# Kernel tuning notes

Measured on AMD Instinct MI355X. Metric: run time of the kernel, lower is better.

## Reference

```python
import jax, jax.numpy as jnp
import numpy as np

N, E = 50000, 400000
HID, EDGE, NRBF = 128, 16, 32
CUTOFF = 5.0
EPS = 1e-8


def setup_inputs() -> dict:
    key = jax.random.key(0)
    ks = jax.random.split(key, 16)
    s = lambda fan_in: 1.0 / np.sqrt(fan_in)
    mlp_in = 3 * HID + NRBF + EDGE  # 432
    return {
        "h": jax.random.normal(ks[0], (N, HID), jnp.float32),
        "vec": jax.random.normal(ks[1], (N, 3, HID), jnp.float32),
        "coord": jax.random.normal(ks[2], (N, 3), jnp.float32),
        "edge_index": jax.random.randint(ks[3], (2, E), 0, N, jnp.int32),
        "edge_attr": jax.random.normal(ks[4], (E, EDGE), jnp.float32),
        "Wvp": jax.random.normal(ks[5], (HID, 3 * HID), jnp.float32) * s(HID),
        "W1": jax.random.normal(ks[6], (mlp_in, HID), jnp.float32) * s(mlp_in),
        "b1": jnp.zeros((HID,), jnp.float32),
        "W2": jax.random.normal(ks[7], (HID, HID), jnp.float32) * s(HID),
        "b2": jnp.zeros((HID,), jnp.float32),
        "W3": jax.random.normal(ks[8], (HID, 3 * HID), jnp.float32) * s(HID),
        "b3": jnp.zeros((3 * HID,), jnp.float32),
        "Wop": jax.random.normal(ks[9], (HID, 3 * HID), jnp.float32) * s(HID),
        "bop": jnp.zeros((3 * HID,), jnp.float32),
    }


def _rbf(d):
    # Gaussian smearing: centers on linspace(0, cutoff, n_rbf)
    offsets = jnp.linspace(0.0, CUTOFF, NRBF, dtype=d.dtype)
    coeff = -0.5 / (offsets[1] - offsets[0]) ** 2
    return jnp.exp(coeff * (d[:, None] - offsets) ** 2)  # [E, NRBF]


def reference(h, vec, coord, edge_index, edge_attr,
              Wvp, W1, b1, W2, b2, W3, b3, Wop, bop):
    row, col = edge_index[0], edge_index[1]
    x_ij = coord[row] - coord[col]                          # [E,3]
    d = jnp.sqrt(jnp.sum(x_ij * x_ij, axis=-1) + EPS)       # stable_norm
    d_ij = _rbf(d)                                          # [E,NRBF]

    vecp = jnp.einsum('nvh,hk->nvk', vec, Wvp)              # [N,3,3H]
    vec1, vec2, vec3 = jnp.split(vecp, 3, axis=-1)          # each [N,3,H]
    vec_dot = jnp.sum(vec1 * vec2, axis=1)                  # [N,H]

    cross = jnp.sum(vec1[row] * vec2[col], axis=1)          # [E,H]
    mlp_in = jnp.concatenate([h[row], h[col], d_ij, cross, edge_attr], axis=-1)
    x = jax.nn.silu(mlp_in @ W1 + b1)
    x = jax.nn.silu(x @ W2 + b2)
    msg = x @ W3 + b3                                       # [E,3H]
    msg_h, msg_v, msg_x = jnp.split(msg, 3, axis=1)

    h_aggr = jax.ops.segment_sum(msg_h, row, num_segments=N)           # [N,H]
    vec_msg = vec3[col] * msg_v[:, None, :] + msg_x[:, None, :] * x_ij[:, :, None]
    vec_aggr = jax.ops.segment_sum(vec_msg, row, num_segments=N)       # [N,3,H]

    o = h_aggr @ Wop + bop
    o1, o2, o3 = jnp.split(o, 3, axis=1)
    dh = vec_dot * o2 + o3
    dvec = vec3 * o1[:, None, :] + vec_aggr
    return dh, dvec
```

## Files before the change

### kernel.cpp

```cpp
#include <hip/hip_runtime.h>
#include <math.h>

constexpr int NN    = 50000;
constexpr int NE    = 400000;
constexpr int HID   = 128;

constexpr size_t OFF_VECP = 0;
constexpr size_t OFF_HAGG = 57600000;
constexpr size_t OFF_HW   = 64000000;
constexpr size_t OFF_WT   = 83200000;
constexpr size_t OFF_PERM = 83421184;
constexpr size_t OFF_DEG  = 83821184;
constexpr size_t OFF_CUR  = 83871184;
constexpr size_t WS_FLOATS = 83921184;

constexpr size_t O_HWH = 0;
constexpr size_t O_HWL = 32768;
constexpr size_t O_W1H = 65536;
constexpr size_t O_W1L = 90112;
constexpr size_t O_W2H = 114688;
constexpr size_t O_W2L = 131072;
constexpr size_t O_W3H = 147456;
constexpr size_t O_W3L = 196608;
constexpr size_t O_VPH = 245760;
constexpr size_t O_VPL = 294912;
constexpr size_t O_OPH = 344064;
constexpr size_t O_OPL = 393216;

typedef __attribute__((ext_vector_type(8))) short short8;
typedef __attribute__((ext_vector_type(4))) float f32x4;

__device__ __forceinline__ short f2bf_rne(float f) {
    unsigned u = __float_as_uint(f);
    u += 0x7fffu + ((u >> 16) & 1u);
    return (short)(u >> 16);
}
__device__ __forceinline__ float bf2f(short h) {
    return __uint_as_float(((unsigned)(unsigned short)h) << 16);
}
__device__ __forceinline__ void split8(const float* t, short8& ah, short8& al) {
#pragma unroll
    for (int j = 0; j < 8; ++j) {
        short hi = f2bf_rne(t[j]);
        ah[j] = hi;
        al[j] = f2bf_rne(t[j] - bf2f(hi));
    }
}
__device__ __forceinline__ f32x4 mfma4(short8 ah, short8 al, short8 bh, short8 bl, f32x4 c) {
    c = __builtin_amdgcn_mfma_f32_16x16x32_bf16(ah, bh, c, 0, 0, 0);
    c = __builtin_amdgcn_mfma_f32_16x16x32_bf16(al, bh, c, 0, 0, 0);
    c = __builtin_amdgcn_mfma_f32_16x16x32_bf16(ah, bl, c, 0, 0, 0);
    c = __builtin_amdgcn_mfma_f32_16x16x32_bf16(al, bl, c, 0, 0, 0);
    return c;
}

#define VLOAD8(dst, src) do { \
    *(float4*)&(dst)[0] = *(const float4*)(src); \
    *(float4*)&(dst)[4] = *(const float4*)((src) + 4); } while (0)

__global__ void misc_kernel(const float* __restrict__ W1, const float* __restrict__ W2,
                            const float* __restrict__ W3, const float* __restrict__ Wvp,
                            const float* __restrict__ Wop, short* __restrict__ wt,
                            const int* __restrict__ eidx, int* __restrict__ deg,
                            float* __restrict__ hagg, float* __restrict__ dvec)
{
    const int bid = blockIdx.x;
    const int idx = bid * 256 + threadIdx.x;
    {
        int n = idx >> 7, k = idx & 127;
        hagg[idx] = 0.f;
        size_t db = (size_t)n * 384 + k;
        dvec[db] = 0.f; dvec[db + 128] = 0.f; dvec[db + 256] = 0.f;
    }
    if (bid < 864) {
        float v; size_t oh, ol;
        if (idx < 32768) {
            int j = idx >> 7, k = idx & 127;
            v = (j < 128) ? W1[(size_t)k * 128 + j] : W1[(size_t)(128 + k) * 128 + (j - 128)];
            oh = O_HWH + idx; ol = O_HWL + idx;
        } else if (idx < 57344) {
            int l = idx - 32768; int n = l / 192, k = l - n * 192;
            int r = (k < 128) ? (288 + k) : (k < 160) ? (256 + k - 128) : (k < 176) ? (416 + k - 160) : -1;
            v = (r < 0) ? 0.f : W1[(size_t)r * 128 + n];
            oh = O_W1H + l; ol = O_W1L + l;
        } else if (idx < 73728) {
            int l = idx - 57344; int n = l >> 7, k = l & 127;
            v = W2[(size_t)k * 128 + n];
            oh = O_W2H + l; ol = O_W2L + l;
        } else if (idx < 122880) {
            int l = idx - 73728; int n = l >> 7, k = l & 127;
            v = W3[(size_t)k * 384 + n];
            oh = O_W3H + l; ol = O_W3L + l;
        } else if (idx < 172032) {
            int l = idx - 122880; int n = l >> 7, k = l & 127;
            v = Wvp[(size_t)k * 384 + n];
            oh = O_VPH + l; ol = O_VPL + l;
        } else {
            int l = idx - 172032; int n = l >> 7, k = l & 127;
            v = Wop[(size_t)k * 384 + n];
            oh = O_OPH + l; ol = O_OPL + l;
        }
        short hi = f2bf_rne(v);
        wt[oh] = hi;
        wt[ol] = f2bf_rne(v - bf2f(hi));
    }
    if (bid < 1563 && idx < NE)
        atomicAdd(&deg[eidx[idx]], 1);
}

__global__ void __launch_bounds__(1024)
sort_scan(const int* __restrict__ deg, int* __restrict__ cursor)
{
    __shared__ int part[1024];
    const int tid = threadIdx.x;
    const int base = tid * 49;
    int s = 0;
#pragma unroll 7
    for (int j = 0; j < 49; ++j) {
        int i = base + j;
        if (i < NN) s += deg[i];
    }
    part[tid] = s;
    __syncthreads();
    for (int off = 1; off < 1024; off <<= 1) {
        int v = (tid >= off) ? part[tid - off] : 0;
        __syncthreads();
        part[tid] += v;
        __syncthreads();
    }
    int run = part[tid] - s;
    for (int j = 0; j < 49; ++j) {
        int i = base + j;
        if (i < NN) { cursor[i] = run; run += deg[i]; }
    }
}

__global__ void sort_scatter(const int* __restrict__ eidx, int* __restrict__ cursor,
                             int* __restrict__ perm)
{
    int e = blockIdx.x * 256 + threadIdx.x;
    if (e < NE) {
        int pos = atomicAdd(&cursor[eidx[e]], 1);
        perm[pos] = e;
    }
}

template<int NT>
__global__ void __launch_bounds__(256, 3)
gemm_node(const float* __restrict__ A, int M,
          const short* __restrict__ wh, const short* __restrict__ wl,
          float* __restrict__ C, const float* __restrict__ bias)
{
    const int N = NT * 64;
    const int tid = threadIdx.x, wave = tid >> 6, lane = tid & 63;
    const int m = lane & 15, kg = lane >> 4;
    const int gm0 = blockIdx.x * 32;
    const int nb = wave * NT * 16;
    const f32x4 zf = {0.f, 0.f, 0.f, 0.f};
    f32x4 acc[2][NT];
#pragma unroll
    for (int mt = 0; mt < 2; ++mt)
#pragma unroll
        for (int tt = 0; tt < NT; ++tt) acc[mt][tt] = zf;

    for (int ks = 0; ks < 4; ++ks) {
        short8 ah[2], al[2];
#pragma unroll
        for (int mt = 0; mt < 2; ++mt) {
            int r = gm0 + mt * 16 + m;
            if (r >= M) r = M - 1;
            float tmp[8];
            VLOAD8(tmp, A + (size_t)r * 128 + ks * 32 + kg * 8);
            split8(tmp, ah[mt], al[mt]);
        }
#pragma unroll
        for (int tt = 0; tt < NT; ++tt) {
            size_t wo = (size_t)(nb + tt * 16 + m) * 128 + ks * 32 + kg * 8;
            short8 bh = *(const short8*)(wh + wo);
            short8 bl = *(const short8*)(wl + wo);
#pragma unroll
            for (int mt = 0; mt < 2; ++mt)
                acc[mt][tt] = mfma4(ah[mt], al[mt], bh, bl, acc[mt][tt]);
        }
    }
    float bv[NT];
#pragma unroll
    for (int tt = 0; tt < NT; ++tt) bv[tt] = bias ? bias[nb + tt * 16 + m] : 0.f;
#pragma unroll
    for (int mt = 0; mt < 2; ++mt)
#pragma unroll
        for (int r = 0; r < 4; ++r) {
            int row = gm0 + mt * 16 + kg * 4 + r;
            if (row < M) {
#pragma unroll
                for (int tt = 0; tt < NT; ++tt)
                    C[(size_t)row * N + nb + tt * 16 + m] = acc[mt][tt][r] + bv[tt];
            }
        }
}

__global__ void __launch_bounds__(256, 3)
gemm_fin(const float* __restrict__ hagg, const float* __restrict__ vecp,
         const short* __restrict__ wh, const short* __restrict__ wl,
         const float* __restrict__ bop, float* __restrict__ dh,
         float* __restrict__ dvec, int M)
{
    const int tid = threadIdx.x, wave = tid >> 6, lane = tid & 63;
    const int m = lane & 15, kg = lane >> 4;
    const int gm0 = blockIdx.x * 32;
    const int nb = wave * 32;
    const f32x4 zf = {0.f, 0.f, 0.f, 0.f};
    f32x4 acc[2][6];
#pragma unroll
    for (int mt = 0; mt < 2; ++mt)
#pragma unroll
        for (int t = 0; t < 6; ++t) acc[mt][t] = zf;

    for (int ks = 0; ks < 4; ++ks) {
        short8 ah[2], al[2];
#pragma unroll
        for (int mt = 0; mt < 2; ++mt) {
            int r = gm0 + mt * 16 + m;
            if (r >= M) r = M - 1;
            float tmp[8];
            VLOAD8(tmp, hagg + (size_t)r * 128 + ks * 32 + kg * 8);
            split8(tmp, ah[mt], al[mt]);
        }
#pragma unroll
        for (int seg = 0; seg < 3; ++seg)
#pragma unroll
            for (int tt = 0; tt < 2; ++tt) {
                size_t wo = (size_t)(seg * 128 + nb + tt * 16 + m) * 128 + ks * 32 + kg * 8;
                short8 bh = *(const short8*)(wh + wo);
                short8 bl = *(const short8*)(wl + wo);
#pragma unroll
                for (int mt = 0; mt < 2; ++mt)
                    acc[mt][seg * 2 + tt] = mfma4(ah[mt], al[mt], bh, bl, acc[mt][seg * 2 + tt]);
            }
    }
    float bo[3][2];
#pragma unroll
    for (int seg = 0; seg < 3; ++seg)
#pragma unroll
        for (int tt = 0; tt < 2; ++tt) bo[seg][tt] = bop[seg * 128 + nb + tt * 16 + m];

#pragma unroll
    for (int mt = 0; mt < 2; ++mt)
#pragma unroll
        for (int r = 0; r < 4; ++r) {
            int row = gm0 + mt * 16 + kg * 4 + r;
            if (row >= M) continue;
            size_t b = (size_t)row * 1152;
#pragma unroll
            for (int tt = 0; tt < 2; ++tt) {
                int k = nb + tt * 16 + m;
                float o1 = acc[mt][0 * 2 + tt][r] + bo[0][tt];
                float o2 = acc[mt][1 * 2 + tt][r] + bo[1][tt];
                float o3 = acc[mt][2 * 2 + tt][r] + bo[2][tt];
                float vd = vecp[b + k]       * vecp[b + 128 + k]
                         + vecp[b + 384 + k] * vecp[b + 512 + k]
                         + vecp[b + 768 + k] * vecp[b + 896 + k];
                dh[(size_t)row * 128 + k] = vd * o2 + o3;
                size_t db = (size_t)row * 384 + k;
                dvec[db]       += vecp[b + 256 + k]  * o1;
                dvec[db + 128] += vecp[b + 640 + k]  * o1;
                dvec[db + 256] += vecp[b + 1024 + k] * o1;
            }
        }
}

__global__ void __launch_bounds__(256, 4)
edge_kernel(const float* __restrict__ vecp, const float* __restrict__ hw,
            const float* __restrict__ coord, const int* __restrict__ eidx,
            const float* __restrict__ eattr, const short* __restrict__ wt,
            const int* __restrict__ perm,
            const float* __restrict__ b1, const float* __restrict__ b2,
            const float* __restrict__ b3,
            float* __restrict__ hagg, float* __restrict__ dvec)
{
    __shared__ __align__(16) unsigned char smem[34816];
    short (*abh)[40]  = (short(*)[40])(&smem[0]);
    short (*abl)[40]  = (short(*)[40])(&smem[5120]);
    short (*xh)[136]  = (short(*)[136])(&smem[0]);
    short (*xl)[136]  = (short(*)[136])(&smem[17408]);
    __shared__ int   s_row[64], s_col[64], s_es[64];
    __shared__ float s_xij[64][3];
    __shared__ float s_d[64];

    const int tid = threadIdx.x;
    const int wave = tid >> 6, lane = tid & 63;
    const int m = lane & 15, kg = lane >> 4;
    const int nb = wave * 32;
    const int eb = blockIdx.x * 64;
    const int be = tid >> 2;
    const int bq = (tid & 3) * 8;

    if (tid < 64) {
        int es = perm[eb + tid];
        int r = eidx[es], c = eidx[NE + es];
        s_es[tid] = es; s_row[tid] = r; s_col[tid] = c;
        float x0 = coord[r * 3 + 0] - coord[c * 3 + 0];
        float x1 = coord[r * 3 + 1] - coord[c * 3 + 1];
        float x2 = coord[r * 3 + 2] - coord[c * 3 + 2];
        s_xij[tid][0] = x0; s_xij[tid][1] = x1; s_xij[tid][2] = x2;
        s_d[tid] = sqrtf(x0 * x0 + x1 * x1 + x2 * x2 + 1e-8f);
    }
    __syncthreads();

    const f32x4 zf = {0.f, 0.f, 0.f, 0.f};
    const float delta = 5.0f / 31.0f;
    const float coeff = -0.5f / (delta * delta);
    const int brow = s_row[be], bcol = s_col[be], bes = s_es[be];

    float pA[8], pB[8], pC[8], pD[8], pE[8], pF[8];
    auto issue = [&](int ks) {
        if (ks < 4) {
            int kk = ks * 32 + bq;
            const float* vr = vecp + (size_t)brow * 1152 + kk;
            const float* vc = vecp + (size_t)bcol * 1152 + 128 + kk;
            VLOAD8(pA, vr);       VLOAD8(pB, vc);
            VLOAD8(pC, vr + 384); VLOAD8(pD, vc + 384);
            VLOAD8(pE, vr + 768); VLOAD8(pF, vc + 768);
        } else if (ks == 5) {
            if (bq < 16) VLOAD8(pA, eattr + (size_t)bes * 16 + bq);
        }
    };
    auto commit = [&](int ks) {
        float tmp[8];
        if (ks < 4) {
#pragma unroll
            for (int j = 0; j < 8; ++j)
                tmp[j] = pA[j] * pB[j] + pC[j] * pD[j] + pE[j] * pF[j];
        } else if (ks == 4) {
            float dd = s_d[be];
#pragma unroll
            for (int j = 0; j < 8; ++j) {
                float x = dd - (float)(bq + j) * delta;
                tmp[j] = __expf(coeff * x * x);
            }
        } else {
#pragma unroll
            for (int j = 0; j < 8; ++j) tmp[j] = (bq < 16) ? pA[j] : 0.f;
        }
        short8 sh, sl; split8(tmp, sh, sl);
        *(short8*)&abh[be][bq] = sh;
        *(short8*)&abl[be][bq] = sl;
    };

    f32x4 acc[4][2];
#pragma unroll
    for (int mt = 0; mt < 4; ++mt) { acc[mt][0] = zf; acc[mt][1] = zf; }

    issue(0); commit(0);
    __syncthreads();
    for (int ks = 0; ks < 6; ++ks) {
        if (ks < 5) issue(ks + 1);
        short8 ah4[4], al4[4];
#pragma unroll
        for (int mt = 0; mt < 4; ++mt) {
            ah4[mt] = *(const short8*)&abh[mt * 16 + m][kg * 8];
            al4[mt] = *(const short8*)&abl[mt * 16 + m][kg * 8];
        }
#pragma unroll
        for (int tt = 0; tt < 2; ++tt) {
            size_t wo = (size_t)(nb + tt * 16 + m) * 192 + ks * 32 + kg * 8;
            short8 bh = *(const short8*)(wt + O_W1H + wo);
            short8 bl = *(const short8*)(wt + O_W1L + wo);
#pragma unroll
            for (int mt = 0; mt < 4; ++mt)
                acc[mt][tt] = mfma4(ah4[mt], al4[mt], bh, bl, acc[mt][tt]);
        }
        __syncthreads();
        if (ks < 5) { commit(ks + 1); __syncthreads(); }
    }

    {
        float b1v[2] = { b1[nb + m], b1[nb + 16 + m] };
#pragma unroll
        for (int mt = 0; mt < 4; ++mt) {
            float hb[4][4];
#pragma unroll
            for (int r = 0; r < 4; ++r) {
                int e = mt * 16 + kg * 4 + r;
                const float* hr = hw + (size_t)s_row[e] * 256;
                const float* hc = hw + (size_t)s_col[e] * 256 + 128;
                hb[r][0] = hr[nb + m];      hb[r][1] = hc[nb + m];
                hb[r][2] = hr[nb + 16 + m]; hb[r][3] = hc[nb + 16 + m];
            }
#pragma unroll
            for (int r = 0; r < 4; ++r) {
                int e = mt * 16 + kg * 4 + r;
#pragma unroll
                for (int tt = 0; tt < 2; ++tt) {
                    int n = nb + tt * 16 + m;
                    float v = acc[mt][tt][r] + hb[r][tt * 2] + hb[r][tt * 2 + 1] + b1v[tt];
                    float sv = v * __builtin_amdgcn_rcpf(1.f + __expf(-v));
                    short hi = f2bf_rne(sv);
                    xh[e][n] = hi;
                    xl[e][n] = f2bf_rne(sv - bf2f(hi));
                }
            }
        }
    }
    __syncthreads();

#pragma unroll
    for (int mt = 0; mt < 4; ++mt) { acc[mt][0] = zf; acc[mt][1] = zf; }
    for (int ks = 0; ks < 4; ++ks) {
        short8 ah4[4], al4[4];
#pragma unroll
        for (int mt = 0; mt < 4; ++mt) {
            ah4[mt] = *(const short8*)&xh[mt * 16 + m][ks * 32 + kg * 8];
            al4[mt] = *(const short8*)&xl[mt * 16 + m][ks * 32 + kg * 8];
        }
#pragma unroll
        for (int tt = 0; tt < 2; ++tt) {
            size_t wo = (size_t)(nb + tt * 16 + m) * 128 + ks * 32 + kg * 8;
            short8 bh = *(const short8*)(wt + O_W2H + wo);
            short8 bl = *(const short8*)(wt + O_W2L + wo);
#pragma unroll
            for (int mt = 0; mt < 4; ++mt)
                acc[mt][tt] = mfma4(ah4[mt], al4[mt], bh, bl, acc[mt][tt]);
        }
    }
    {
        float b2v[2] = { b2[nb + m], b2[nb + 16 + m] };
#pragma unroll
        for (int mt = 0; mt < 4; ++mt)
#pragma unroll
            for (int tt = 0; tt < 2; ++tt)
#pragma unroll
                for (int r = 0; r < 4; ++r) {
                    float v = acc[mt][tt][r] + b2v[tt];
                    acc[mt][tt][r] = v * __builtin_amdgcn_rcpf(1.f + __expf(-v));
                }
    }
    __syncthreads();
#pragma unroll
    for (int mt = 0; mt < 4; ++mt)
#pragma unroll
        for (int tt = 0; tt < 2; ++tt)
#pragma unroll
            for (int r = 0; r < 4; ++r) {
                int e = mt * 16 + kg * 4 + r;
                int n = nb + tt * 16 + m;
                float sv = acc[mt][tt][r];
                short hi = f2bf_rne(sv);
                xh[e][n] = hi;
                xl[e][n] = f2bf_rne(sv - bf2f(hi));
            }
    __syncthreads();

    float msgv[4][2][4];
    for (int c = 0; c < 3; ++c) {
        f32x4 a3[4][2];
#pragma unroll
        for (int mt = 0; mt < 4; ++mt) { a3[mt][0] = zf; a3[mt][1] = zf; }
        for (int ks = 0; ks < 4; ++ks) {
            short8 ah4[4], al4[4];
#pragma unroll
            for (int mt = 0; mt < 4; ++mt) {
                ah4[mt] = *(const short8*)&xh[mt * 16 + m][ks * 32 + kg * 8];
                al4[mt] = *(const short8*)&xl[mt * 16 + m][ks * 32 + kg * 8];
            }
#pragma unroll
            for (int tt = 0; tt < 2; ++tt) {
                size_t wo = (size_t)(c * 128 + nb + tt * 16 + m) * 128 + ks * 32 + kg * 8;
                short8 bh = *(const short8*)(wt + O_W3H + wo);
                short8 bl = *(const short8*)(wt + O_W3L + wo);
#pragma unroll
                for (int mt = 0; mt < 4; ++mt)
                    a3[mt][tt] = mfma4(ah4[mt], al4[mt], bh, bl, a3[mt][tt]);
            }
        }
        float bv[2] = { b3[c * 128 + nb + m], b3[c * 128 + nb + 16 + m] };
        const int n0 = nb + m, n1 = nb + 16 + m;
        if (c == 0) {
            int cur = s_row[kg * 4];
            float s0 = 0.f, s1 = 0.f;
#pragma unroll
            for (int mt = 0; mt < 4; ++mt)
#pragma unroll
                for (int r = 0; r < 4; ++r) {
                    int rr = s_row[mt * 16 + kg * 4 + r];
                    float v0 = a3[mt][0][r] + bv[0];
                    float v1 = a3[mt][1][r] + bv[1];
                    if (rr != cur) {
                        atomicAdd(&hagg[(size_t)cur * 128 + n0], s0);
                        atomicAdd(&hagg[(size_t)cur * 128 + n1], s1);
                        cur = rr; s0 = 0.f; s1 = 0.f;
                    }
                    s0 += v0; s1 += v1;
                }
            atomicAdd(&hagg[(size_t)cur * 128 + n0], s0);
            atomicAdd(&hagg[(size_t)cur * 128 + n1], s1);
        } else if (c == 1) {
#pragma unroll
            for (int mt = 0; mt < 4; ++mt)
#pragma unroll
                for (int tt = 0; tt < 2; ++tt)
#pragma unroll
                    for (int r = 0; r < 4; ++r)
                        msgv[mt][tt][r] = a3[mt][tt][r] + bv[tt];
        } else {
            int cur = s_row[kg * 4];
            float sd[6] = {0.f, 0.f, 0.f, 0.f, 0.f, 0.f};
#pragma unroll
            for (int mt = 0; mt < 4; ++mt) {
                float v3b[4][6];
#pragma unroll
                for (int r = 0; r < 4; ++r) {
                    int e = mt * 16 + kg * 4 + r;
                    const float* v3 = vecp + (size_t)s_col[e] * 1152 + 256;
                    v3b[r][0] = v3[n0]; v3b[r][1] = v3[384 + n0]; v3b[r][2] = v3[768 + n0];
                    v3b[r][3] = v3[n1]; v3b[r][4] = v3[384 + n1]; v3b[r][5] = v3[768 + n1];
                }
#pragma unroll
                for (int r = 0; r < 4; ++r) {
                    int e = mt * 16 + kg * 4 + r;
                    int rr = s_row[e];
                    if (rr != cur) {
                        float* dst = dvec + (size_t)cur * 384;
                        atomicAdd(dst + n0,       sd[0]);
                        atomicAdd(dst + 128 + n0, sd[1]);
                        atomicAdd(dst + 256 + n0, sd[2]);
                        atomicAdd(dst + n1,       sd[3]);
                        atomicAdd(dst + 128 + n1, sd[4]);
                        atomicAdd(dst + 256 + n1, sd[5]);
                        cur = rr;
#pragma unroll
                        for (int q = 0; q < 6; ++q) sd[q] = 0.f;
                    }
                    const float xj0 = s_xij[e][0], xj1 = s_xij[e][1], xj2 = s_xij[e][2];
                    float mx0 = a3[mt][0][r] + bv[0], mx1 = a3[mt][1][r] + bv[1];
                    float mv0 = msgv[mt][0][r],       mv1 = msgv[mt][1][r];
                    sd[0] += v3b[r][0] * mv0 + xj0 * mx0;
                    sd[1] += v3b[r][1] * mv0 + xj1 * mx0;
                    sd[2] += v3b[r][2] * mv0 + xj2 * mx0;
                    sd[3] += v3b[r][3] * mv1 + xj0 * mx1;
                    sd[4] += v3b[r][4] * mv1 + xj1 * mx1;
                    sd[5] += v3b[r][5] * mv1 + xj2 * mx1;
                }
            }
            float* dst = dvec + (size_t)cur * 384;
            atomicAdd(dst + n0,       sd[0]);
            atomicAdd(dst + 128 + n0, sd[1]);
            atomicAdd(dst + 256 + n0, sd[2]);
            atomicAdd(dst + n1,       sd[3]);
            atomicAdd(dst + 128 + n1, sd[4]);
            atomicAdd(dst + 256 + n1, sd[5]);
        }
    }
}

extern "C" void kernel_launch(void* const* d_in, const int* in_sizes, int n_in,
                              void* d_out, int out_size, void* d_ws, size_t ws_size,
                              hipStream_t stream)
{
    const float* h     = (const float*)d_in[0];
    const float* vec   = (const float*)d_in[1];
    const float* coord = (const float*)d_in[2];
    const int*   eidx  = (const int*)  d_in[3];
    const float* eattr = (const float*)d_in[4];
    const float* Wvp   = (const float*)d_in[5];
    const float* W1    = (const float*)d_in[6];
    const float* b1    = (const float*)d_in[7];
    const float* W2    = (const float*)d_in[8];
    const float* b2    = (const float*)d_in[9];
    const float* W3    = (const float*)d_in[10];
    const float* b3    = (const float*)d_in[11];
    const float* Wop   = (const float*)d_in[12];
    const float* bop   = (const float*)d_in[13];

    if (ws_size < WS_FLOATS * sizeof(float)) return;

    float* ws   = (float*)d_ws;
    float* vecp = ws + OFF_VECP;
    float* hagg = ws + OFF_HAGG;
    float* hw   = ws + OFF_HW;
    short* wt   = (short*)(ws + OFF_WT);
    int*   perm = (int*)(ws + OFF_PERM);
    int*   deg  = (int*)(ws + OFF_DEG);
    int*   cur  = (int*)(ws + OFF_CUR);
    float* dh   = (float*)d_out;
    float* dvec = (float*)d_out + (size_t)NN * HID;

    dim3 b256(256);
    hipMemsetAsync(deg, 0, NN * sizeof(int), stream);
    misc_kernel<<<25000, b256, 0, stream>>>(W1, W2, W3, Wvp, Wop, wt, eidx, deg, hagg, dvec);
    sort_scan<<<1, 1024, 0, stream>>>(deg, cur);
    sort_scatter<<<1563, b256, 0, stream>>>(eidx, cur, perm);
    gemm_node<6><<<4688, b256, 0, stream>>>(vec, 150000, wt + O_VPH, wt + O_VPL, vecp, nullptr);
    gemm_node<4><<<1563, b256, 0, stream>>>(h, 50000, wt + O_HWH, wt + O_HWL, hw, nullptr);
    edge_kernel<<<6250, b256, 0, stream>>>(vecp, hw, coord, eidx, eattr, wt, perm,
                                           b1, b2, b3, hagg, dvec);
    gemm_fin<<<1563, b256, 0, stream>>>(hagg, vecp, wt + O_OPH, wt + O_OPL, bop, dh, dvec, 50000);
}
```

Before: 1.340 ms.

## Halve edge tile to 32 edges per block and double-buffer first-layer staging

Result: slower. 1.668 ms (+24.5%).

```diff
diff --git a/kernel.cpp b/kernel.cpp
--- a/kernel.cpp
+++ b/kernel.cpp
@@ -28,6 +28,7 @@
 constexpr size_t O_OPL = 393216;
 
 typedef __attribute__((ext_vector_type(8))) short short8;
+typedef __attribute__((ext_vector_type(4))) short s16x4;
 typedef __attribute__((ext_vector_type(4))) float f32x4;
 
 __device__ __forceinline__ short f2bf_rne(float f) {
@@ -41,6 +42,14 @@
 __device__ __forceinline__ void split8(const float* t, short8& ah, short8& al) {
 #pragma unroll
     for (int j = 0; j < 8; ++j) {
+        short hi = f2bf_rne(t[j]);
+        ah[j] = hi;
+        al[j] = f2bf_rne(t[j] - bf2f(hi));
+    }
+}
+__device__ __forceinline__ void split4(const float* t, s16x4& ah, s16x4& al) {
+#pragma unroll
+    for (int j = 0; j < 4; ++j) {
         short hi = f2bf_rne(t[j]);
         ah[j] = hi;
         al[j] = f2bf_rne(t[j] - bf2f(hi));
@@ -57,6 +66,8 @@
 #define VLOAD8(dst, src) do { \
     *(float4*)&(dst)[0] = *(const float4*)(src); \
     *(float4*)&(dst)[4] = *(const float4*)((src) + 4); } while (0)
+#define VLOAD4(dst, src) do { \
+    *(float4*)&(dst)[0] = *(const float4*)(src); } while (0)
 
 __global__ void misc_kernel(const float* __restrict__ W1, const float* __restrict__ W2,
                             const float* __restrict__ W3, const float* __restrict__ Wvp,
@@ -269,7 +280,7 @@
         }
 }
 
-__global__ void __launch_bounds__(256, 4)
+__global__ void __launch_bounds__(256, 8)
 edge_kernel(const float* __restrict__ vecp, const float* __restrict__ hw,
             const float* __restrict__ coord, const int* __restrict__ eidx,
             const float* __restrict__ eattr, const short* __restrict__ wt,
@@ -278,24 +289,22 @@
             const float* __restrict__ b3,
             float* __restrict__ hagg, float* __restrict__ dvec)
 {
-    __shared__ __align__(16) unsigned char smem[34816];
-    short (*abh)[40]  = (short(*)[40])(&smem[0]);
-    short (*abl)[40]  = (short(*)[40])(&smem[5120]);
-    short (*xh)[136]  = (short(*)[136])(&smem[0]);
-    short (*xl)[136]  = (short(*)[136])(&smem[17408]);
-    __shared__ int   s_row[64], s_col[64], s_es[64];
-    __shared__ float s_xij[64][3];
-    __shared__ float s_d[64];
+    __shared__ __align__(16) unsigned char smem[17408];
+    short (*xh)[136] = (short(*)[136])(&smem[0]);
+    short (*xl)[136] = (short(*)[136])(&smem[8704]);
+    __shared__ int   s_row[32], s_col[32], s_es[32];
+    __shared__ float s_xij[32][3];
+    __shared__ float s_d[32];
 
     const int tid = threadIdx.x;
     const int wave = tid >> 6, lane = tid & 63;
     const int m = lane & 15, kg = lane >> 4;
     const int nb = wave * 32;
-    const int eb = blockIdx.x * 64;
-    const int be = tid >> 2;
-    const int bq = (tid & 3) * 8;
-
-    if (tid < 64) {
+    const int eb = blockIdx.x * 32;
+    const int be = tid >> 3;
+    const int bq = (tid & 7) * 4;
+
+    if (tid < 32) {
         int es = perm[eb + tid];
         int r = eidx[es], c = eidx[NE + es];
         s_es[tid] = es; s_row[tid] = r; s_col[tid] = c;
@@ -312,54 +321,58 @@
     const float coeff = -0.5f / (delta * delta);
     const int brow = s_row[be], bcol = s_col[be], bes = s_es[be];
 
-    float pA[8], pB[8], pC[8], pD[8], pE[8], pF[8];
+    float pA[4], pB[4], pC[4], pD[4], pE[4], pF[4];
     auto issue = [&](int ks) {
         if (ks < 4) {
             int kk = ks * 32 + bq;
             const float* vr = vecp + (size_t)brow * 1152 + kk;
             const float* vc = vecp + (size_t)bcol * 1152 + 128 + kk;
-            VLOAD8(pA, vr);       VLOAD8(pB, vc);
-            VLOAD8(pC, vr + 384); VLOAD8(pD, vc + 384);
-            VLOAD8(pE, vr + 768); VLOAD8(pF, vc + 768);
+            VLOAD4(pA, vr);       VLOAD4(pB, vc);
+            VLOAD4(pC, vr + 384); VLOAD4(pD, vc + 384);
+            VLOAD4(pE, vr + 768); VLOAD4(pF, vc + 768);
         } else if (ks == 5) {
-            if (bq < 16) VLOAD8(pA, eattr + (size_t)bes * 16 + bq);
+            if (bq < 16) VLOAD4(pA, eattr + (size_t)bes * 16 + bq);
         }
     };
-    auto commit = [&](int ks) {
-        float tmp[8];
+    auto commit = [&](int ks, int buf) {
+        short (*cabh)[40] = (short(*)[40])(&smem[(size_t)buf * 2560]);
+        short (*cabl)[40] = (short(*)[40])(&smem[5120 + (size_t)buf * 2560]);
+        float tmp[4];
         if (ks < 4) {
 #pragma unroll
-            for (int j = 0; j < 8; ++j)
+            for (int j = 0; j < 4; ++j)
                 tmp[j] = pA[j] * pB[j] + pC[j] * pD[j] + pE[j] * pF[j];
         } else if (ks == 4) {
             float dd = s_d[be];
 #pragma unroll
-            for (int j = 0; j < 8; ++j) {
+            for (int j = 0; j < 4; ++j) {
                 float x = dd - (float)(bq + j) * delta;
                 tmp[j] = __expf(coeff * x * x);
             }
         } else {
 #pragma unroll
-            for (int j = 0; j < 8; ++j) tmp[j] = (bq < 16) ? pA[j] : 0.f;
-        }
-        short8 sh, sl; split8(tmp, sh, sl);
-        *(short8*)&abh[be][bq] = sh;
-        *(short8*)&abl[be][bq] = sl;
+            for (int j = 0; j < 4; ++j) tmp[j] = (bq < 16) ? pA[j] : 0.f;
+        }
+        s16x4 sh, sl; split4(tmp, sh, sl);
+        *(s16x4*)&cabh[be][bq] = sh;
+        *(s16x4*)&cabl[be][bq] = sl;
     };
 
-    f32x4 acc[4][2];
-#pragma unroll
-    for (int mt = 0; mt < 4; ++mt) { acc[mt][0] = zf; acc[mt][1] = zf; }
-
-    issue(0); commit(0);
+    f32x4 acc[2][2];
+#pragma unroll
+    for (int mt = 0; mt < 2; ++mt) { acc[mt][0] = zf; acc[mt][1] = zf; }
+
+    issue(0); commit(0, 0);
     __syncthreads();
     for (int ks = 0; ks < 6; ++ks) {
         if (ks < 5) issue(ks + 1);
-        short8 ah4[4], al4[4];
-#pragma unroll
-        for (int mt = 0; mt < 4; ++mt) {
-            ah4[mt] = *(const short8*)&abh[mt * 16 + m][kg * 8];
-            al4[mt] = *(const short8*)&abl[mt * 16 + m][kg * 8];
+        const short (*rabh)[40] = (const short(*)[40])(&smem[(size_t)(ks & 1) * 2560]);
+        const short (*rabl)[40] = (const short(*)[40])(&smem[5120 + (size_t)(ks & 1) * 2560]);
+        short8 ah4[2], al4[2];
+#pragma unroll
+        for (int mt = 0; mt < 2; ++mt) {
+            ah4[mt] = *(const short8*)&rabh[mt * 16 + m][kg * 8];
+            al4[mt] = *(const short8*)&rabl[mt * 16 + m][kg * 8];
         }
 #pragma unroll
         for (int tt = 0; tt < 2; ++tt) {
@@ -367,17 +380,17 @@
             short8 bh = *(const short8*)(wt + O_W1H + wo);
             short8 bl = *(const short8*)(wt + O_W1L + wo);
 #pragma unroll
-            for (int mt = 0; mt < 4; ++mt)
+            for (int mt = 0; mt < 2; ++mt)
                 acc[mt][tt] = mfma4(ah4[mt], al4[mt], bh, bl, acc[mt][tt]);
         }
+        if (ks < 5) commit(ks + 1, (ks + 1) & 1);
         __syncthreads();
-        if (ks < 5) { commit(ks + 1); __syncthreads(); }
     }
 
     {
         float b1v[2] = { b1[nb + m], b1[nb + 16 + m] };
 #pragma unroll
-        for (int mt = 0; mt < 4; ++mt) {
+        for (int mt = 0; mt < 2; ++mt) {
             float hb[4][4];
 #pragma unroll
             for (int r = 0; r < 4; ++r) {
@@ -405,11 +418,11 @@
     __syncthreads();
 
 #pragma unroll
-    for (int mt = 0; mt < 4; ++mt) { acc[mt][0] = zf; acc[mt][1] = zf; }
+    for (int mt = 0; mt < 2; ++mt) { acc[mt][0] = zf; acc[mt][1] = zf; }
     for (int ks = 0; ks < 4; ++ks) {
-        short8 ah4[4], al4[4];
-#pragma unroll
-        for (int mt = 0; mt < 4; ++mt) {
+        short8 ah4[2], al4[2];
+#pragma unroll
+        for (int mt = 0; mt < 2; ++mt) {
             ah4[mt] = *(const short8*)&xh[mt * 16 + m][ks * 32 + kg * 8];
             al4[mt] = *(const short8*)&xl[mt * 16 + m][ks * 32 + kg * 8];
         }
@@ -419,14 +432,14 @@
             short8 bh = *(const short8*)(wt + O_W2H + wo);
             short8 bl = *(const short8*)(wt + O_W2L + wo);
 #pragma unroll
-            for (int mt = 0; mt < 4; ++mt)
+            for (int mt = 0; mt < 2; ++mt)
                 acc[mt][tt] = mfma4(ah4[mt], al4[mt], bh, bl, acc[mt][tt]);
         }
     }
     {
         float b2v[2] = { b2[nb + m], b2[nb + 16 + m] };
 #pragma unroll
-        for (int mt = 0; mt < 4; ++mt)
+        for (int mt = 0; mt < 2; ++mt)
 #pragma unroll
             for (int tt = 0; tt < 2; ++tt)
 #pragma unroll
@@ -437,7 +450,7 @@
     }
     __syncthreads();
 #pragma unroll
-    for (int mt = 0; mt < 4; ++mt)
+    for (int mt = 0; mt < 2; ++mt)
 #pragma unroll
         for (int tt = 0; tt < 2; ++tt)
 #pragma unroll
@@ -451,15 +464,15 @@
             }
     __syncthreads();
 
-    float msgv[4][2][4];
+    float msgv[2][2][4];
     for (int c = 0; c < 3; ++c) {
-        f32x4 a3[4][2];
-#pragma unroll
-        for (int mt = 0; mt < 4; ++mt) { a3[mt][0] = zf; a3[mt][1] = zf; }
+        f32x4 a3[2][2];
+#pragma unroll
+        for (int mt = 0; mt < 2; ++mt) { a3[mt][0] = zf; a3[mt][1] = zf; }
         for (int ks = 0; ks < 4; ++ks) {
-            short8 ah4[4], al4[4];
-#pragma unroll
-            for (int mt = 0; mt < 4; ++mt) {
+            short8 ah4[2], al4[2];
+#pragma unroll
+            for (int mt = 0; mt < 2; ++mt) {
                 ah4[mt] = *(const short8*)&xh[mt * 16 + m][ks * 32 + kg * 8];
                 al4[mt] = *(const short8*)&xl[mt * 16 + m][ks * 32 + kg * 8];
             }
@@ -469,7 +482,7 @@
                 short8 bh = *(const short8*)(wt + O_W3H + wo);
                 short8 bl = *(const short8*)(wt + O_W3L + wo);
 #pragma unroll
-                for (int mt = 0; mt < 4; ++mt)
+                for (int mt = 0; mt < 2; ++mt)
                     a3[mt][tt] = mfma4(ah4[mt], al4[mt], bh, bl, a3[mt][tt]);
             }
         }
@@ -479,7 +492,7 @@
             int cur = s_row[kg * 4];
             float s0 = 0.f, s1 = 0.f;
 #pragma unroll
-            for (int mt = 0; mt < 4; ++mt)
+            for (int mt = 0; mt < 2; ++mt)
 #pragma unroll
                 for (int r = 0; r < 4; ++r) {
                     int rr = s_row[mt * 16 + kg * 4 + r];
@@ -496,7 +509,7 @@
             atomicAdd(&hagg[(size_t)cur * 128 + n1], s1);
         } else if (c == 1) {
 #pragma unroll
-            for (int mt = 0; mt < 4; ++mt)
+            for (int mt = 0; mt < 2; ++mt)
 #pragma unroll
                 for (int tt = 0; tt < 2; ++tt)
 #pragma unroll
@@ -506,7 +519,7 @@
             int cur = s_row[kg * 4];
             float sd[6] = {0.f, 0.f, 0.f, 0.f, 0.f, 0.f};
 #pragma unroll
-            for (int mt = 0; mt < 4; ++mt) {
+            for (int mt = 0; mt < 2; ++mt) {
                 float v3b[4][6];
 #pragma unroll
                 for (int r = 0; r < 4; ++r) {
@@ -592,7 +605,7 @@
     sort_scatter<<<1563, b256, 0, stream>>>(eidx, cur, perm);
     gemm_node<6><<<4688, b256, 0, stream>>>(vec, 150000, wt + O_VPH, wt + O_VPL, vecp, nullptr);
     gemm_node<4><<<1563, b256, 0, stream>>>(h, 50000, wt + O_HWH, wt + O_HWL, hw, nullptr);
-    edge_kernel<<<6250, b256, 0, stream>>>(vecp, hw, coord, eidx, eattr, wt, perm,
-                                           b1, b2, b3, hagg, dvec);
+    edge_kernel<<<12500, b256, 0, stream>>>(vecp, hw, coord, eidx, eattr, wt, perm,
+                                            b1, b2, b3, hagg, dvec);
     gemm_fin<<<1563, b256, 0, stream>>>(hagg, vecp, wt + O_OPH, wt + O_OPL, bop, dh, dvec, 50000);
 }
```

## Store gathered node features as bf16 bundle, double-buffer edge LDS, remap blocks per XCD

Applied to the files above, without the earlier changes.

Result: faster. 1.289 ms (-3.8%).

```diff
diff --git a/kernel.cpp b/kernel.cpp
--- a/kernel.cpp
+++ b/kernel.cpp
@@ -5,9 +5,9 @@
 constexpr int NE    = 400000;
 constexpr int HID   = 128;
 
-constexpr size_t OFF_VECP = 0;
-constexpr size_t OFF_HAGG = 57600000;
-constexpr size_t OFF_HW   = 64000000;
+constexpr size_t OFF_VECP12 = 0;
+constexpr size_t OFF_BUN  = 38400000;
+constexpr size_t OFF_HAGG = 64000000;
 constexpr size_t OFF_WT   = 83200000;
 constexpr size_t OFF_PERM = 83421184;
 constexpr size_t OFF_DEG  = 83821184;
@@ -145,23 +145,21 @@
     }
 }
 
-template<int NT>
 __global__ void __launch_bounds__(256, 3)
-gemm_node(const float* __restrict__ A, int M,
-          const short* __restrict__ wh, const short* __restrict__ wl,
-          float* __restrict__ C, const float* __restrict__ bias)
-{
-    const int N = NT * 64;
+gemm_vp(const float* __restrict__ A, int M,
+        const short* __restrict__ wh, const short* __restrict__ wl,
+        float* __restrict__ vecp12, short* __restrict__ bun)
+{
     const int tid = threadIdx.x, wave = tid >> 6, lane = tid & 63;
     const int m = lane & 15, kg = lane >> 4;
     const int gm0 = blockIdx.x * 32;
-    const int nb = wave * NT * 16;
+    const int nb = wave * 96;
     const f32x4 zf = {0.f, 0.f, 0.f, 0.f};
-    f32x4 acc[2][NT];
+    f32x4 acc[2][6];
 #pragma unroll
     for (int mt = 0; mt < 2; ++mt)
 #pragma unroll
-        for (int tt = 0; tt < NT; ++tt) acc[mt][tt] = zf;
+        for (int tt = 0; tt < 6; ++tt) acc[mt][tt] = zf;
 
     for (int ks = 0; ks < 4; ++ks) {
         short8 ah[2], al[2];
@@ -174,7 +172,7 @@
             split8(tmp, ah[mt], al[mt]);
         }
 #pragma unroll
-        for (int tt = 0; tt < NT; ++tt) {
+        for (int tt = 0; tt < 6; ++tt) {
             size_t wo = (size_t)(nb + tt * 16 + m) * 128 + ks * 32 + kg * 8;
             short8 bh = *(const short8*)(wh + wo);
             short8 bl = *(const short8*)(wl + wo);
@@ -183,24 +181,86 @@
                 acc[mt][tt] = mfma4(ah[mt], al[mt], bh, bl, acc[mt][tt]);
         }
     }
-    float bv[NT];
-#pragma unroll
-    for (int tt = 0; tt < NT; ++tt) bv[tt] = bias ? bias[nb + tt * 16 + m] : 0.f;
 #pragma unroll
     for (int mt = 0; mt < 2; ++mt)
 #pragma unroll
         for (int r = 0; r < 4; ++r) {
             int row = gm0 + mt * 16 + kg * 4 + r;
-            if (row < M) {
-#pragma unroll
-                for (int tt = 0; tt < NT; ++tt)
-                    C[(size_t)row * N + nb + tt * 16 + m] = acc[mt][tt][r] + bv[tt];
+            if (row >= M) continue;
+            int n = row / 3, v = row - n * 3;
+            size_t fb = (size_t)n * 768 + (size_t)v * 256;
+            size_t b2 = (size_t)n * 1024 + (size_t)v * 128;
+            size_t b3 = (size_t)n * 1024 + 384 + (size_t)v * 128;
+#pragma unroll
+            for (int tt = 0; tt < 6; ++tt) {
+                int col = nb + tt * 16 + m;
+                float val = acc[mt][tt][r];
+                int seg = col >> 7, k = col & 127;
+                if (seg == 0) {
+                    vecp12[fb + k] = val;
+                } else if (seg == 1) {
+                    vecp12[fb + 128 + k] = val;
+                    bun[b2 + k] = f2bf_rne(val);
+                } else {
+                    bun[b3 + k] = f2bf_rne(val);
+                }
             }
         }
 }
 
 __global__ void __launch_bounds__(256, 3)
-gemm_fin(const float* __restrict__ hagg, const float* __restrict__ vecp,
+gemm_hw(const float* __restrict__ A, int M,
+        const short* __restrict__ wh, const short* __restrict__ wl,
+        short* __restrict__ bun)
+{
+    const int tid = threadIdx.x, wave = tid >> 6, lane = tid & 63;
+    const int m = lane & 15, kg = lane >> 4;
+    const int gm0 = blockIdx.x * 32;
+    const int nb = wave * 64;
+    const f32x4 zf = {0.f, 0.f, 0.f, 0.f};
+    f32x4 acc[2][4];
+#pragma unroll
+    for (int mt = 0; mt < 2; ++mt)
+#pragma unroll
+        for (int tt = 0; tt < 4; ++tt) acc[mt][tt] = zf;
+
+    for (int ks = 0; ks < 4; ++ks) {
+        short8 ah[2], al[2];
+#pragma unroll
+        for (int mt = 0; mt < 2; ++mt) {
+            int r = gm0 + mt * 16 + m;
+            if (r >= M) r = M - 1;
+            float tmp[8];
+            VLOAD8(tmp, A + (size_t)r * 128 + ks * 32 + kg * 8);
+            split8(tmp, ah[mt], al[mt]);
+        }
+#pragma unroll
+        for (int tt = 0; tt < 4; ++tt) {
+            size_t wo = (size_t)(nb + tt * 16 + m) * 128 + ks * 32 + kg * 8;
+            short8 bh = *(const short8*)(wh + wo);
+            short8 bl = *(const short8*)(wl + wo);
+#pragma unroll
+            for (int mt = 0; mt < 2; ++mt)
+                acc[mt][tt] = mfma4(ah[mt], al[mt], bh, bl, acc[mt][tt]);
+        }
+    }
+#pragma unroll
+    for (int mt = 0; mt < 2; ++mt)
+#pragma unroll
+        for (int r = 0; r < 4; ++r) {
+            int row = gm0 + mt * 16 + kg * 4 + r;
+            if (row >= M) continue;
+#pragma unroll
+            for (int tt = 0; tt < 4; ++tt) {
+                int col = nb + tt * 16 + m;
+                bun[(size_t)row * 1024 + 768 + col] = f2bf_rne(acc[mt][tt][r]);
+            }
+        }
+}
+
+__global__ void __launch_bounds__(256, 3)
+gemm_fin(const float* __restrict__ hagg, const float* __restrict__ vecp12,
+         const short* __restrict__ bun,
          const short* __restrict__ wh, const short* __restrict__ wl,
          const float* __restrict__ bop, float* __restrict__ dh,
          float* __restrict__ dvec, int M)
@@ -250,27 +310,28 @@
         for (int r = 0; r < 4; ++r) {
             int row = gm0 + mt * 16 + kg * 4 + r;
             if (row >= M) continue;
-            size_t b = (size_t)row * 1152;
+            size_t b = (size_t)row * 768;
+            size_t bb = (size_t)row * 1024 + 384;
 #pragma unroll
             for (int tt = 0; tt < 2; ++tt) {
                 int k = nb + tt * 16 + m;
                 float o1 = acc[mt][0 * 2 + tt][r] + bo[0][tt];
                 float o2 = acc[mt][1 * 2 + tt][r] + bo[1][tt];
                 float o3 = acc[mt][2 * 2 + tt][r] + bo[2][tt];
-                float vd = vecp[b + k]       * vecp[b + 128 + k]
-                         + vecp[b + 384 + k] * vecp[b + 512 + k]
-                         + vecp[b + 768 + k] * vecp[b + 896 + k];
+                float vd = vecp12[b + k]       * vecp12[b + 128 + k]
+                         + vecp12[b + 256 + k] * vecp12[b + 384 + k]
+                         + vecp12[b + 512 + k] * vecp12[b + 640 + k];
                 dh[(size_t)row * 128 + k] = vd * o2 + o3;
                 size_t db = (size_t)row * 384 + k;
-                dvec[db]       += vecp[b + 256 + k]  * o1;
-                dvec[db + 128] += vecp[b + 640 + k]  * o1;
-                dvec[db + 256] += vecp[b + 1024 + k] * o1;
+                dvec[db]       += bf2f(bun[bb + k])       * o1;
+                dvec[db + 128] += bf2f(bun[bb + 128 + k]) * o1;
+                dvec[db + 256] += bf2f(bun[bb + 256 + k]) * o1;
             }
         }
 }
 
 __global__ void __launch_bounds__(256, 4)
-edge_kernel(const float* __restrict__ vecp, const float* __restrict__ hw,
+edge_kernel(const float* __restrict__ vecp12, const short* __restrict__ bun,
             const float* __restrict__ coord, const int* __restrict__ eidx,
             const float* __restrict__ eattr, const short* __restrict__ wt,
             const int* __restrict__ perm,
@@ -279,19 +340,22 @@
             float* __restrict__ hagg, float* __restrict__ dvec)
 {
     __shared__ __align__(16) unsigned char smem[34816];
-    short (*abh)[40]  = (short(*)[40])(&smem[0]);
-    short (*abl)[40]  = (short(*)[40])(&smem[5120]);
     short (*xh)[136]  = (short(*)[136])(&smem[0]);
     short (*xl)[136]  = (short(*)[136])(&smem[17408]);
     __shared__ int   s_row[64], s_col[64], s_es[64];
     __shared__ float s_xij[64][3];
     __shared__ float s_d[64];
 
+    const int nwg = gridDim.x;
+    const int q8 = nwg >> 3, r8 = nwg & 7;
+    const int xcd = blockIdx.x & 7, loc = blockIdx.x >> 3;
+    const int lb = (xcd < r8 ? xcd * (q8 + 1) : r8 * (q8 + 1) + (xcd - r8) * q8) + loc;
+
     const int tid = threadIdx.x;
     const int wave = tid >> 6, lane = tid & 63;
     const int m = lane & 15, kg = lane >> 4;
     const int nb = wave * 32;
-    const int eb = blockIdx.x * 64;
+    const int eb = lb * 64;
     const int be = tid >> 2;
     const int bq = (tid & 3) * 8;
 
@@ -312,25 +376,29 @@
     const float coeff = -0.5f / (delta * delta);
     const int brow = s_row[be], bcol = s_col[be], bes = s_es[be];
 
-    float pA[8], pB[8], pC[8], pD[8], pE[8], pF[8];
+    float pA[8], pC[8], pE[8];
+    short8 bB, bD, bF;
     auto issue = [&](int ks) {
         if (ks < 4) {
             int kk = ks * 32 + bq;
-            const float* vr = vecp + (size_t)brow * 1152 + kk;
-            const float* vc = vecp + (size_t)bcol * 1152 + 128 + kk;
-            VLOAD8(pA, vr);       VLOAD8(pB, vc);
-            VLOAD8(pC, vr + 384); VLOAD8(pD, vc + 384);
-            VLOAD8(pE, vr + 768); VLOAD8(pF, vc + 768);
+            const float* vr = vecp12 + (size_t)brow * 768 + kk;
+            const short* vc = bun + (size_t)bcol * 1024 + kk;
+            VLOAD8(pA, vr); VLOAD8(pC, vr + 256); VLOAD8(pE, vr + 512);
+            bB = *(const short8*)(vc);
+            bD = *(const short8*)(vc + 128);
+            bF = *(const short8*)(vc + 256);
         } else if (ks == 5) {
             if (bq < 16) VLOAD8(pA, eattr + (size_t)bes * 16 + bq);
         }
     };
-    auto commit = [&](int ks) {
+    auto commit = [&](int ks, int buf) {
+        short (*cabh)[40] = (short(*)[40])(&smem[(size_t)buf * 5120]);
+        short (*cabl)[40] = (short(*)[40])(&smem[10240 + (size_t)buf * 5120]);
         float tmp[8];
         if (ks < 4) {
 #pragma unroll
             for (int j = 0; j < 8; ++j)
-                tmp[j] = pA[j] * pB[j] + pC[j] * pD[j] + pE[j] * pF[j];
+                tmp[j] = pA[j] * bf2f(bB[j]) + pC[j] * bf2f(bD[j]) + pE[j] * bf2f(bF[j]);
         } else if (ks == 4) {
             float dd = s_d[be];
 #pragma unroll
@@ -343,23 +411,25 @@
             for (int j = 0; j < 8; ++j) tmp[j] = (bq < 16) ? pA[j] : 0.f;
         }
         short8 sh, sl; split8(tmp, sh, sl);
-        *(short8*)&abh[be][bq] = sh;
-        *(short8*)&abl[be][bq] = sl;
+        *(short8*)&cabh[be][bq] = sh;
+        *(short8*)&cabl[be][bq] = sl;
     };
 
     f32x4 acc[4][2];
 #pragma unroll
     for (int mt = 0; mt < 4; ++mt) { acc[mt][0] = zf; acc[mt][1] = zf; }
 
-    issue(0); commit(0);
+    issue(0); commit(0, 0);
     __syncthreads();
     for (int ks = 0; ks < 6; ++ks) {
         if (ks < 5) issue(ks + 1);
+        const short (*rabh)[40] = (const short(*)[40])(&smem[(size_t)(ks & 1) * 5120]);
+        const short (*rabl)[40] = (const short(*)[40])(&smem[10240 + (size_t)(ks & 1) * 5120]);
         short8 ah4[4], al4[4];
 #pragma unroll
         for (int mt = 0; mt < 4; ++mt) {
-            ah4[mt] = *(const short8*)&abh[mt * 16 + m][kg * 8];
-            al4[mt] = *(const short8*)&abl[mt * 16 + m][kg * 8];
+            ah4[mt] = *(const short8*)&rabh[mt * 16 + m][kg * 8];
+            al4[mt] = *(const short8*)&rabl[mt * 16 + m][kg * 8];
         }
 #pragma unroll
         for (int tt = 0; tt < 2; ++tt) {
@@ -370,8 +440,8 @@
             for (int mt = 0; mt < 4; ++mt)
                 acc[mt][tt] = mfma4(ah4[mt], al4[mt], bh, bl, acc[mt][tt]);
         }
+        if (ks < 5) commit(ks + 1, (ks + 1) & 1);
         __syncthreads();
-        if (ks < 5) { commit(ks + 1); __syncthreads(); }
     }
 
     {
@@ -382,10 +452,10 @@
 #pragma unroll
             for (int r = 0; r < 4; ++r) {
                 int e = mt * 16 + kg * 4 + r;
-                const float* hr = hw + (size_t)s_row[e] * 256;
-                const float* hc = hw + (size_t)s_col[e] * 256 + 128;
-                hb[r][0] = hr[nb + m];      hb[r][1] = hc[nb + m];
-                hb[r][2] = hr[nb + 16 + m]; hb[r][3] = hc[nb + 16 + m];
+                const short* hr = bun + (size_t)s_row[e] * 1024 + 768;
+                const short* hc = bun + (size_t)s_col[e] * 1024 + 896;
+                hb[r][0] = bf2f(hr[nb + m]);      hb[r][1] = bf2f(hc[nb + m]);
+                hb[r][2] = bf2f(hr[nb + 16 + m]); hb[r][3] = bf2f(hc[nb + 16 + m]);
             }
 #pragma unroll
             for (int r = 0; r < 4; ++r) {
@@ -511,9 +581,9 @@
 #pragma unroll
                 for (int r = 0; r < 4; ++r) {
                     int e = mt * 16 + kg * 4 + r;
-                    const float* v3 = vecp + (size_t)s_col[e] * 1152 + 256;
-                    v3b[r][0] = v3[n0]; v3b[r][1] = v3[384 + n0]; v3b[r][2] = v3[768 + n0];
-                    v3b[r][3] = v3[n1]; v3b[r][4] = v3[384 + n1]; v3b[r][5] = v3[768 + n1];
+                    const short* v3 = bun + (size_t)s_col[e] * 1024 + 384;
+                    v3b[r][0] = bf2f(v3[n0]); v3b[r][1] = bf2f(v3[128 + n0]); v3b[r][2] = bf2f(v3[256 + n0]);
+                    v3b[r][3] = bf2f(v3[n1]); v3b[r][4] = bf2f(v3[128 + n1]); v3b[r][5] = bf2f(v3[256 + n1]);
                 }
 #pragma unroll
                 for (int r = 0; r < 4; ++r) {
@@ -574,25 +644,26 @@
 
     if (ws_size < WS_FLOATS * sizeof(float)) return;
 
-    float* ws   = (float*)d_ws;
-    float* vecp = ws + OFF_VECP;
-    float* hagg = ws + OFF_HAGG;
-    float* hw   = ws + OFF_HW;
-    short* wt   = (short*)(ws + OFF_WT);
-    int*   perm = (int*)(ws + OFF_PERM);
-    int*   deg  = (int*)(ws + OFF_DEG);
-    int*   cur  = (int*)(ws + OFF_CUR);
-    float* dh   = (float*)d_out;
-    float* dvec = (float*)d_out + (size_t)NN * HID;
+    float* ws     = (float*)d_ws;
+    float* vecp12 = ws + OFF_VECP12;
+    short* bun    = (short*)(ws + OFF_BUN);
+    float* hagg   = ws + OFF_HAGG;
+    short* wt     = (short*)(ws + OFF_WT);
+    int*   perm   = (int*)(ws + OFF_PERM);
+    int*   deg    = (int*)(ws + OFF_DEG);
+    int*   cur    = (int*)(ws + OFF_CUR);
+    float* dh     = (float*)d_out;
+    float* dvec   = (float*)d_out + (size_t)NN * HID;
 
     dim3 b256(256);
     hipMemsetAsync(deg, 0, NN * sizeof(int), stream);
     misc_kernel<<<25000, b256, 0, stream>>>(W1, W2, W3, Wvp, Wop, wt, eidx, deg, hagg, dvec);
     sort_scan<<<1, 1024, 0, stream>>>(deg, cur);
     sort_scatter<<<1563, b256, 0, stream>>>(eidx, cur, perm);
-    gemm_node<6><<<4688, b256, 0, stream>>>(vec, 150000, wt + O_VPH, wt + O_VPL, vecp, nullptr);
-    gemm_node<4><<<1563, b256, 0, stream>>>(h, 50000, wt + O_HWH, wt + O_HWL, hw, nullptr);
-    edge_kernel<<<6250, b256, 0, stream>>>(vecp, hw, coord, eidx, eattr, wt, perm,
+    gemm_vp<<<4688, b256, 0, stream>>>(vec, 150000, wt + O_VPH, wt + O_VPL, vecp12, bun);
+    gemm_hw<<<1563, b256, 0, stream>>>(h, 50000, wt + O_HWH, wt + O_HWL, bun);
+    edge_kernel<<<6250, b256, 0, stream>>>(vecp12, bun, coord, eidx, eattr, wt, perm,
                                            b1, b2, b3, hagg, dvec);
-    gemm_fin<<<1563, b256, 0, stream>>>(hagg, vecp, wt + O_OPH, wt + O_OPL, bop, dh, dvec, 50000);
-}
+    gemm_fin<<<1563, b256, 0, stream>>>(hagg, vecp12, bun, wt + O_OPH, wt + O_OPL,
+                                        bop, dh, dvec, 50000);
+}
```
